# Optimization experiments

Measured on AMD Instinct MI355X. Metric: run time of the kernel, lower is better.

The kernel has to match this reference:

```python
import jax, jax.numpy as jnp
import numpy as np

B, E, H, D = 1, 400000, 8, 32
N_NODES = 50000


def setup_inputs() -> dict:
    key = jax.random.key(0)
    kq, kk, ka, ki = jax.random.split(key, 4)
    q = jax.random.normal(kq, (B, E, H, D), dtype=jnp.float32)
    k = jax.random.normal(kk, (B, E, H, D), dtype=jnp.float32)
    # glorot on [1, H, 2D]: std = sqrt(2 / (fan_in + fan_out)) ~ sqrt(2/(2D))
    attn = jax.random.normal(ka, (1, H, 2 * D), dtype=jnp.float32) * np.sqrt(2.0 / (2 * D))
    index = jnp.sort(jax.random.randint(ki, (E,), 0, N_NODES, dtype=jnp.int32))
    return {"q": q, "k": k, "attn": attn, "index": index, "n_nodes": N_NODES}


def _segment_softmax(score, index, num_segments):
    # score: [B, E, H]; softmax over edges sharing the same segment id.
    s = jnp.moveaxis(score, 1, 0)                      # [E, B, H]
    seg_max = jax.ops.segment_max(s, index, num_segments=num_segments)  # [N, B, H]
    s = jnp.exp(s - seg_max[index])                    # gather max per edge
    seg_sum = jax.ops.segment_sum(s, index, num_segments=num_segments)  # [N, B, H]
    out = s / seg_sum[index]
    return jnp.moveaxis(out, 0, 1)                     # [B, E, H]


def reference(q, k, attn, index, n_nodes):
    Dh = q.shape[-1]
    a = attn[None]                                     # [1, 1, H, 2D] (batchlize branch)
    a_q, a_k = a[..., :Dh], a[..., Dh:]
    # equivalent to relu(((cat([q,k],-1) * attn).sum(-1)) without materializing concat
    score = jax.nn.relu(jnp.einsum('behd,xyhd->beh', q, a_q)
                        + jnp.einsum('behd,xyhd->beh', k, a_k))  # [B, E, H]
    return _segment_softmax(score, index, n_nodes)     # dropout p=0.0 is identity
```

## Files before the change

kernel.cpp:

```cpp
#include <hip/hip_runtime.h>

static constexpr int kH = 8;
static constexpr int kD = 32;
static constexpr int kNN = 50000;
static constexpr int kRun = 8;

typedef float f4 __attribute__((ext_vector_type(4)));

__device__ __forceinline__ float dot8(const f4 a, const f4 b, const f4 c, const f4 d) {
  return a.x * b.x + a.y * b.y + a.z * b.z + a.w * b.w
       + c.x * d.x + c.y * d.y + c.z * d.z + c.w * d.w;
}

__global__ void __launch_bounds__(256) score_exp_kernel(
    const float* __restrict__ q, const float* __restrict__ k,
    const float* __restrict__ attn, const int* __restrict__ index,
    float* __restrict__ out, float* __restrict__ node_sum, int nedges) {
  const int lane = threadIdx.x & 63;
  const int h = lane >> 3;
  const int sub = lane & 7;

  const f4 aq = *reinterpret_cast<const f4*>(attn + h * (2 * kD) + sub * 4);
  const f4 ak = *reinterpret_cast<const f4*>(attn + h * (2 * kD) + kD + sub * 4);

  const int wave   = (blockIdx.x * blockDim.x + threadIdx.x) >> 6;
  const int nwaves = (gridDim.x * blockDim.x) >> 6;

  const f4* qv = reinterpret_cast<const f4*>(q);
  const f4* kv = reinterpret_cast<const f4*>(k);

  for (int base = wave * kRun; base < nedges; base += nwaves * kRun) {
    const int e_end = min(base + kRun, nedges);
    int cur = index[base];
    float acc = 0.0f;
    #pragma unroll 1
    for (int e = base; e < e_end; ++e) {
      const f4 q4 = __builtin_nontemporal_load(qv + (size_t)e * 64 + lane);
      const f4 k4 = __builtin_nontemporal_load(kv + (size_t)e * 64 + lane);
      const int node = index[e];

      float p = dot8(q4, aq, k4, ak);
      p += __shfl_xor(p, 1);
      p += __shfl_xor(p, 2);
      p += __shfl_xor(p, 4);
      const float v = __expf(fmaxf(p, 0.0f));

      if (sub == 0) out[(size_t)e * kH + h] = v;

      if (node != cur) {
        if (sub == 0) atomicAdd(node_sum + (size_t)cur * kH + h, acc);
        acc = 0.0f;
        cur = node;
      }
      acc += v;
    }
    if (sub == 0) atomicAdd(node_sum + (size_t)cur * kH + h, acc);
  }
}

__global__ void __launch_bounds__(256) norm_kernel(
    const int* __restrict__ index, const float* __restrict__ node_sum,
    float* __restrict__ out, int nedges) {
  int e = blockIdx.x * blockDim.x + threadIdx.x;
  if (e >= nedges) return;
  int node = index[e];
  const f4 s0 = *reinterpret_cast<const f4*>(node_sum + (size_t)node * kH);
  const f4 s1 = *reinterpret_cast<const f4*>(node_sum + (size_t)node * kH + 4);
  f4* o = reinterpret_cast<f4*>(out + (size_t)e * kH);
  f4 v0 = o[0], v1 = o[1];
  v0.x /= s0.x; v0.y /= s0.y; v0.z /= s0.z; v0.w /= s0.w;
  v1.x /= s1.x; v1.y /= s1.y; v1.z /= s1.z; v1.w /= s1.w;
  o[0] = v0; o[1] = v1;
}

extern "C" void kernel_launch(void* const* d_in, const int* in_sizes, int n_in,
                              void* d_out, int out_size, void* d_ws, size_t ws_size,
                              hipStream_t stream) {
  const float* q    = (const float*)d_in[0];
  const float* k    = (const float*)d_in[1];
  const float* attn = (const float*)d_in[2];
  const int* index  = (const int*)d_in[3];

  const int E = in_sizes[3];

  float* out      = (float*)d_out;
  float* node_sum = (float*)d_ws;

  (void)hipMemsetAsync(node_sum, 0, (size_t)kNN * kH * sizeof(float), stream);

  score_exp_kernel<<<2048, 256, 0, stream>>>(q, k, attn, index, out, node_sum, E);

  norm_kernel<<<(E + 255) / 256, 256, 0, stream>>>(index, node_sum, out, E);
}
```

Measured before the change: 161.8 us.

## Fuse segment sum and normalization into one kernel using segment-owning waves

Each wave now takes a contiguous chunk of edges. It skips any segment that began in the previous chunk and finishes its last segment even past the chunk end, so every segment belongs to exactly one wave. The wave computes exp scores, sums each segment locally, then rescales that segment's outputs in place. This removes the memset, the atomics and the separate normalize kernel with its second pass over the index. The costs are a serial read-modify-write rescale loop run by only the sub==0 lanes, and some load imbalance from segment boundaries.

```diff
diff --git a/kernel.cpp b/kernel.cpp
--- a/kernel.cpp
+++ b/kernel.cpp
@@ -2,8 +2,6 @@
 
 static constexpr int kH = 8;
 static constexpr int kD = 32;
-static constexpr int kNN = 50000;
-static constexpr int kRun = 8;
 
 typedef float f4 __attribute__((ext_vector_type(4)));
 
@@ -12,10 +10,10 @@
        + c.x * d.x + c.y * d.y + c.z * d.z + c.w * d.w;
 }
 
-__global__ void __launch_bounds__(256) score_exp_kernel(
+__global__ void __launch_bounds__(256, 8) fused_softmax_kernel(
     const float* __restrict__ q, const float* __restrict__ k,
     const float* __restrict__ attn, const int* __restrict__ index,
-    float* __restrict__ out, float* __restrict__ node_sum, int nedges) {
+    float* __restrict__ out, int nedges) {
   const int lane = threadIdx.x & 63;
   const int h = lane >> 3;
   const int sub = lane & 7;
@@ -26,18 +24,31 @@
   const int wave   = (blockIdx.x * blockDim.x + threadIdx.x) >> 6;
   const int nwaves = (gridDim.x * blockDim.x) >> 6;
 
+  const int cpw = (nedges + nwaves - 1) / nwaves;
+  const int cs = wave * cpw;
+  if (cs >= nedges) return;
+  const int ce = min(cs + cpw, nedges);
+
+  int e = cs;
+  if (cs > 0) {
+    const int prev = index[cs - 1];
+    while (e < ce && index[e] == prev) ++e;
+    if (e >= ce) return;
+  }
+
   const f4* qv = reinterpret_cast<const f4*>(q);
   const f4* kv = reinterpret_cast<const f4*>(k);
 
-  for (int base = wave * kRun; base < nedges; base += nwaves * kRun) {
-    const int e_end = min(base + kRun, nedges);
-    int cur = index[base];
+  int node = index[e];
+  for (;;) {
+    const int ns = e;
     float acc = 0.0f;
+    int nxt;
     #pragma unroll 1
-    for (int e = base; e < e_end; ++e) {
+    do {
       const f4 q4 = __builtin_nontemporal_load(qv + (size_t)e * 64 + lane);
       const f4 k4 = __builtin_nontemporal_load(kv + (size_t)e * 64 + lane);
-      const int node = index[e];
+      nxt = (e + 1 < nedges) ? index[e + 1] : -1;
 
       float p = dot8(q4, aq, k4, ak);
       p += __shfl_xor(p, 1);
@@ -46,31 +57,21 @@
       const float v = __expf(fmaxf(p, 0.0f));
 
       if (sub == 0) out[(size_t)e * kH + h] = v;
+      acc += v;
+      ++e;
+    } while (nxt == node);
 
-      if (node != cur) {
-        if (sub == 0) atomicAdd(node_sum + (size_t)cur * kH + h, acc);
-        acc = 0.0f;
-        cur = node;
+    const float rcp = 1.0f / acc;
+    if (sub == 0) {
+      #pragma unroll 1
+      for (int i = ns; i < e; ++i) {
+        out[(size_t)i * kH + h] *= rcp;
       }
-      acc += v;
     }
-    if (sub == 0) atomicAdd(node_sum + (size_t)cur * kH + h, acc);
+
+    if (nxt < 0 || e >= ce) break;
+    node = nxt;
   }
-}
-
-__global__ void __launch_bounds__(256) norm_kernel(
-    const int* __restrict__ index, const float* __restrict__ node_sum,
-    float* __restrict__ out, int nedges) {
-  int e = blockIdx.x * blockDim.x + threadIdx.x;
-  if (e >= nedges) return;
-  int node = index[e];
-  const f4 s0 = *reinterpret_cast<const f4*>(node_sum + (size_t)node * kH);
-  const f4 s1 = *reinterpret_cast<const f4*>(node_sum + (size_t)node * kH + 4);
-  f4* o = reinterpret_cast<f4*>(out + (size_t)e * kH);
-  f4 v0 = o[0], v1 = o[1];
-  v0.x /= s0.x; v0.y /= s0.y; v0.z /= s0.z; v0.w /= s0.w;
-  v1.x /= s1.x; v1.y /= s1.y; v1.z /= s1.z; v1.w /= s1.w;
-  o[0] = v0; o[1] = v1;
 }
 
 extern "C" void kernel_launch(void* const* d_in, const int* in_sizes, int n_in,
@@ -83,12 +84,7 @@
 
   const int E = in_sizes[3];
 
-  float* out      = (float*)d_out;
-  float* node_sum = (float*)d_ws;
+  float* out = (float*)d_out;
 
-  (void)hipMemsetAsync(node_sum, 0, (size_t)kNN * kH * sizeof(float), stream);
-
-  score_exp_kernel<<<2048, 256, 0, stream>>>(q, k, attn, index, out, node_sum, E);
-
-  norm_kernel<<<(E + 255) / 256, 256, 0, stream>>>(index, node_sum, out, E);
+  fused_softmax_kernel<<<2048, 256, 0, stream>>>(q, k, attn, index, out, E);
 }
```

After: 159.2 us. Within noise of the previous version (-1.6%).
